# Kernel optimization log

Measured on AMD Instinct MI355X. Metric: run time of the kernel, lower is better.

The kernel has to match this reference:

```python
import jax, jax.numpy as jnp
import numpy as np

B, S, D = 4096, 10, 1024

def setup_inputs() -> dict:
    key = jax.random.key(0)
    ks = jax.random.split(key, 8)
    sD = 1.0 / np.sqrt(D)
    s2D = 1.0 / np.sqrt(2 * D)
    sH = 1.0 / np.sqrt(D // 2)
    return {
        "input_1": jax.random.normal(ks[0], (B, S, D), jnp.float32),
        "input_2": jax.random.normal(ks[1], (B, S, D), jnp.float32),
        # mlp_graph: Linear(2D -> D), stored (in, out)
        "Wg": jax.random.uniform(ks[2], (2 * D, D), jnp.float32, -s2D, s2D),
        "bg": jax.random.uniform(ks[3], (D,), jnp.float32, -s2D, s2D),
        # fd: Linear(2D -> D//2)
        "Wfd": jax.random.uniform(ks[4], (2 * D, D // 2), jnp.float32, -s2D, s2D),
        "bfd": jax.random.uniform(ks[5], (D // 2,), jnp.float32, -s2D, s2D),
        # ff: Linear(D//2 -> 1)
        "Wff": jax.random.uniform(ks[6], (D // 2, 1), jnp.float32, -sH, sH),
        "bff": jax.random.uniform(ks[7], (1,), jnp.float32, -sH, sH),
    }

def reference(input_1, input_2, Wg, bg, Wfd, bfd, Wff, bff):
    # graph_match: cross-graph affinity [B, S, T]
    a = jnp.einsum('bsd,btd->bst', input_1, input_2)
    a_x = jax.nn.softmax(a, axis=1)   # softmax over rows (dim=1)
    a_y = jax.nn.softmax(a, axis=0)   # unusual cross-batch softmax (dim=0)
    # attention_x = a_x^T @ input_1 ; attention_y = a_y @ input_2
    attention_x = jnp.einsum('bst,bsd->btd', a_x, input_1)
    attention_y = jnp.einsum('bst,btd->bsd', a_y, input_2)
    output_x = jnp.concatenate([input_1, attention_y], axis=2) @ Wg + bg
    output_y = jnp.concatenate([input_2, attention_x], axis=2) @ Wg + bg
    # training head: last token of each, concat, fd-ReLU-ff-Sigmoid
    o1 = output_x[:, -1, :]
    o2 = output_y[:, -1, :]
    h = jax.nn.relu(jnp.concatenate([o1, o2], axis=1) @ Wfd + bfd)
    logits = jnp.squeeze(h @ Wff + bff, axis=-1)
    return jax.nn.sigmoid(logits)
```

## Files before the change

kernel.cpp:

```cpp
#include <hip/hip_runtime.h>
#include <hip/hip_bf16.h>

#define BATCH 4096
#define SEQ 10
#define DIM 1024
#define TWOD 2048
#define HID 512

typedef __attribute__((ext_vector_type(8))) short bf16x8;
typedef __attribute__((ext_vector_type(4))) float f32x4;

#define OFF_ABF   0ull
#define OFF_OCB   (32ull << 20)
#define OFF_WGT   (48ull << 20)
#define OFF_WFDT  (52ull << 20)
#define OFF_LOG   (54ull << 20)
#define OFF_AROW  (62ull << 20)
#define OFF_STATS (OFF_AROW + 4096ull * 16 * 4)

#define GLOAD_LDS16(g, l)                                                     \
  __builtin_amdgcn_global_load_lds(                                           \
      (const __attribute__((address_space(1))) unsigned int*)(g),             \
      (__attribute__((address_space(3))) unsigned int*)(l), 16, 0, 0)

#define SW(r) (((r) + ((r) >> 2)) & 3)

static __device__ inline void store_bf4(__hip_bfloat16* p, float4 v) {
  ushort4 u;
  __hip_bfloat16 a = __float2bfloat16(v.x), b = __float2bfloat16(v.y),
                 c = __float2bfloat16(v.z), d = __float2bfloat16(v.w);
  u.x = *(unsigned short*)&a; u.y = *(unsigned short*)&b;
  u.z = *(unsigned short*)&c; u.w = *(unsigned short*)&d;
  *(ushort4*)p = u;
}

__global__ __launch_bounds__(256) void k_scores(
    const float* __restrict__ X1, const float* __restrict__ X2,
    __hip_bfloat16* __restrict__ abf, float* __restrict__ arow,
    float* __restrict__ logits) {
  int b = blockIdx.x;
  int tid = threadIdx.x;
  int wave = tid >> 6, lane = tid & 63;
  const float* x1b = X1 + (size_t)b * SEQ * DIM;
  const float* x2b = X2 + (size_t)b * SEQ * DIM;
  __shared__ float sc[20];
  __shared__ float4 xch[4 * 64];
  if (tid == 0) logits[b] = 0.f;

  const float* Abase;
  const float* Brow;
  if (wave == 0)      { Abase = x1b;           Brow = x2b + 9 * DIM; }
  else if (wave == 1) { Abase = x1b + 5 * DIM; Brow = x2b + 9 * DIM; }
  else if (wave == 2) { Abase = x2b;           Brow = x1b + 9 * DIM; }
  else                { Abase = x2b + 5 * DIM; Brow = x1b + 9 * DIM; }

  float4 ra[5][4], rb[4];
#pragma unroll
  for (int i = 0; i < 4; i++)
    rb[i] = *(const float4*)(Brow + i * 256 + lane * 4);
#pragma unroll
  for (int s = 0; s < 5; s++)
#pragma unroll
    for (int i = 0; i < 4; i++)
      ra[s][i] = *(const float4*)(Abase + s * DIM + i * 256 + lane * 4);

  float v[5];
#pragma unroll
  for (int s = 0; s < 5; s++) {
    float4 a4 = ra[s][0] * rb[0] + ra[s][1] * rb[1] + ra[s][2] * rb[2] +
                ra[s][3] * rb[3];
    v[s] = a4.x + a4.y + a4.z + a4.w;
  }
#pragma unroll
  for (int off = 1; off < 64; off <<= 1)
#pragma unroll
    for (int s = 0; s < 5; s++) v[s] += __shfl_xor(v[s], off, 64);

  if (lane == 0) {
    int base = wave * 5;
    sc[base + 0] = v[0]; sc[base + 1] = v[1]; sc[base + 2] = v[2];
    sc[base + 3] = v[3]; sc[base + 4] = v[4];
  }
  __syncthreads();

  if (tid < SEQ) arow[(size_t)b * 16 + tid] = sc[10 + tid];

  float px[SEQ];
#pragma unroll
  for (int s = 0; s < SEQ; s++) px[s] = sc[s];
  float m = -1e30f;
#pragma unroll
  for (int s = 0; s < SEQ; s++) m = fmaxf(m, px[s]);
  float w[SEQ], Z = 0.f;
#pragma unroll
  for (int s = 0; s < SEQ; s++) { w[s] = __expf(px[s] - m); Z += w[s]; }
  float inv = 1.f / Z;

  __hip_bfloat16* rowx1 = abf + (size_t)b * TWOD;
  __hip_bfloat16* rowx2 = abf + (size_t)(BATCH + b) * TWOD;

  if (wave == 1) {
#pragma unroll
    for (int i = 0; i < 4; i++) {
      float4 pb = ra[0][i] * w[5] + ra[1][i] * w[6] + ra[2][i] * w[7] +
                  ra[3][i] * w[8] + ra[4][i] * w[9];
      xch[i * 64 + lane] = pb;
      store_bf4(rowx2 + i * 256 + lane * 4, rb[i]);
    }
  } else if (wave == 2) {
#pragma unroll
    for (int i = 0; i < 4; i++)
      store_bf4(rowx1 + i * 256 + lane * 4, rb[i]);
  }
  __syncthreads();
  if (wave == 0) {
#pragma unroll
    for (int i = 0; i < 4; i++) {
      float4 ax = ra[0][i] * w[0] + ra[1][i] * w[1] + ra[2][i] * w[2] +
                  ra[3][i] * w[3] + ra[4][i] * w[4];
      ax = (ax + xch[i * 64 + lane]) * inv;
      store_bf4(rowx2 + DIM + i * 256 + lane * 4, ax);
    }
  }
}

__global__ __launch_bounds__(256) void k_stats(const float* __restrict__ arow,
                                               float* __restrict__ stats) {
  int t = blockIdx.x;
  int tid = threadIdx.x, lane = tid & 63, wave = tid >> 6;
  __shared__ float wred[4];
  float m = -1e30f;
  for (int b = tid; b < BATCH; b += 256) m = fmaxf(m, arow[(size_t)b * 16 + t]);
  for (int off = 32; off; off >>= 1) m = fmaxf(m, __shfl_down(m, off, 64));
  if (lane == 0) wred[wave] = m;
  __syncthreads();
  m = fmaxf(fmaxf(wred[0], wred[1]), fmaxf(wred[2], wred[3]));
  __syncthreads();
  float z = 0.f;
  for (int b = tid; b < BATCH; b += 256) z += __expf(arow[(size_t)b * 16 + t] - m);
  for (int off = 32; off; off >>= 1) z += __shfl_down(z, off, 64);
  if (lane == 0) wred[wave] = z;
  __syncthreads();
  if (tid == 0) {
    stats[t] = m;
    stats[16 + t] = wred[0] + wred[1] + wred[2] + wred[3];
  }
}

__global__ __launch_bounds__(256) void k_apply_y(const float* __restrict__ X2,
                                                 const float* __restrict__ arow,
                                                 const float* __restrict__ stats,
                                                 __hip_bfloat16* __restrict__ abf) {
  int b = blockIdx.x;
  int wave = threadIdx.x >> 6, lane = threadIdx.x & 63;
  float wy[SEQ];
#pragma unroll
  for (int t = 0; t < SEQ; t++)
    wy[t] = __expf(arow[(size_t)b * 16 + t] - stats[t]) / stats[16 + t];
  const float* x2b = X2 + (size_t)b * SEQ * DIM;
  int d = wave * 256 + lane * 4;
  float4 acc = {0.f, 0.f, 0.f, 0.f};
#pragma unroll
  for (int t = 0; t < SEQ; t++)
    acc += wy[t] * *(const float4*)(x2b + t * DIM + d);
  store_bf4(abf + (size_t)b * TWOD + DIM + d, acc);
}

__global__ __launch_bounds__(256) void k_transpose_both(
    const float* __restrict__ Wg, const float* __restrict__ Wfd,
    __hip_bfloat16* __restrict__ wgt, __hip_bfloat16* __restrict__ wfdt) {
  __shared__ float t[32][33];
  int by = blockIdx.y;
  const float* in;
  __hip_bfloat16* out;
  int C, c0;
  if (by < 32) { in = Wg; out = wgt; C = DIM; c0 = by * 32; }
  else         { in = Wfd; out = wfdt; C = HID; c0 = (by - 32) * 32; }
  int r0 = blockIdx.x * 32;
  int tx = threadIdx.x & 31, ty = threadIdx.x >> 5;
#pragma unroll
  for (int i = 0; i < 4; i++)
    t[ty + 8 * i][tx] = in[(size_t)(r0 + ty + 8 * i) * C + c0 + tx];
  __syncthreads();
#pragma unroll
  for (int i = 0; i < 4; i++)
    out[(size_t)(c0 + ty + 8 * i) * TWOD + r0 + tx] =
        __float2bfloat16(t[tx][ty + 8 * i]);
}

#define G1_BUF  24576
#define G1_BOFF 16384
#define G1_NT   32

__global__ __launch_bounds__(512, 1) void k_gemm1(
    const __hip_bfloat16* __restrict__ A, const __hip_bfloat16* __restrict__ Bt,
    const float* __restrict__ bias, __hip_bfloat16* __restrict__ outb, int K) {
  __shared__ short lds[3 * G1_BUF];
  int tid = threadIdx.x;
  int lane = tid & 63, wave = tid >> 6;
  int flat = blockIdx.x;
  int swz = (flat & 7) * 32 + (flat >> 3);
  int m0 = (swz >> 3) * 256, n0 = (swz & 7) * 128;
  int wr = wave >> 2, wc = wave & 3;
  int g = lane >> 4, r16 = lane & 15;

  int srow = tid >> 3;
  int ss = (tid & 7) ^ (srow & 7);
  const __hip_bfloat16* sa = A + (size_t)(m0 + srow) * K + ss * 8;
  const __hip_bfloat16* sb = Bt + (size_t)(n0 + srow) * K + ss * 8;
  int dA = wave * 512;
  int dB = G1_BOFF + wave * 512;

#define G1_STAGE(kt, c)                                                       \
  {                                                                           \
    const __hip_bfloat16* sak = sa + (kt)*64;                                 \
    const __hip_bfloat16* sbk = sb + (kt)*64;                                 \
    GLOAD_LDS16(sak + 0 * 64 * K, &lds[(c)*G1_BUF + dA + 0 * 4096]);          \
    GLOAD_LDS16(sak + 1 * 64 * K, &lds[(c)*G1_BUF + dA + 1 * 4096]);          \
    GLOAD_LDS16(sak + 2 * 64 * K, &lds[(c)*G1_BUF + dA + 2 * 4096]);          \
    GLOAD_LDS16(sak + 3 * 64 * K, &lds[(c)*G1_BUF + dA + 3 * 4096]);          \
    GLOAD_LDS16(sbk + 0 * 64 * K, &lds[(c)*G1_BUF + dB + 0 * 4096]);          \
    GLOAD_LDS16(sbk + 1 * 64 * K, &lds[(c)*G1_BUF + dB + 1 * 4096]);          \
  }

  f32x4 acc[8][2] = {};

  G1_STAGE(0, 0);
  G1_STAGE(1, 1);
  asm volatile("s_waitcnt vmcnt(6)" ::: "memory");
  __builtin_amdgcn_sched_barrier(0);
  __builtin_amdgcn_s_barrier();
  __builtin_amdgcn_sched_barrier(0);

#pragma unroll 1
  for (int kt = 0; kt < G1_NT; ++kt) {
    int cur = kt - (kt / 3) * 3;
    if (kt + 2 < G1_NT) {
      int nx = (kt + 2) - ((kt + 2) / 3) * 3;
      G1_STAGE(kt + 2, nx);
    }
    const short* bufA = &lds[cur * G1_BUF];
    const short* bufB = &lds[cur * G1_BUF + G1_BOFF];
#pragma unroll
    for (int kk = 0; kk < 2; ++kk) {
      int sr = ((kk * 4 + g) ^ (r16 & 7)) * 8;
      bf16x8 af[8], bfr[2];
#pragma unroll
      for (int mi = 0; mi < 8; mi++)
        af[mi] = *(const bf16x8*)&bufA[(wr * 128 + mi * 16 + r16) * 64 + sr];
#pragma unroll
      for (int ni = 0; ni < 2; ni++)
        bfr[ni] = *(const bf16x8*)&bufB[(wc * 32 + ni * 16 + r16) * 64 + sr];
      __builtin_amdgcn_s_setprio(1);
#pragma unroll
      for (int mi = 0; mi < 8; mi++)
#pragma unroll
        for (int ni = 0; ni < 2; ni++)
          acc[mi][ni] = __builtin_amdgcn_mfma_f32_16x16x32_bf16(
              af[mi], bfr[ni], acc[mi][ni], 0, 0, 0);
      __builtin_amdgcn_s_setprio(0);
    }
    if (kt < G1_NT - 2)
      asm volatile("s_waitcnt vmcnt(6)" ::: "memory");
    else
      asm volatile("s_waitcnt vmcnt(0)" ::: "memory");
    __builtin_amdgcn_sched_barrier(0);
    __builtin_amdgcn_s_barrier();
    __builtin_amdgcn_sched_barrier(0);
  }

#pragma unroll
  for (int mi = 0; mi < 8; mi++) {
#pragma unroll
    for (int ni = 0; ni < 2; ni++) {
#pragma unroll
      for (int r = 0; r < 4; r++) {
        int m = m0 + wr * 128 + mi * 16 + g * 4 + r;
        int n = n0 + wc * 32 + ni * 16 + r16;
        float v = acc[mi][ni][r] + bias[n];
        int om = m & (BATCH - 1);
        int on = n + ((m >> 12) << 10);
        outb[(size_t)om * TWOD + on] = __float2bfloat16(v);
      }
    }
  }
#undef G1_STAGE
}

#define G2_BUF  12288
#define G2_BOFF 8192
#define G2_NT   32

__global__ __launch_bounds__(256) void k_gemm2_final(
    const __hip_bfloat16* __restrict__ A, const __hip_bfloat16* __restrict__ Bt,
    const float* __restrict__ bfd, const float* __restrict__ Wff,
    float* __restrict__ logits, int K) {
  __shared__ short lds[3 * G2_BUF];
  int tid = threadIdx.x;
  int lane = tid & 63, wave = tid >> 6;
  int flat = blockIdx.x;
  int swz = (flat & 7) * 32 + (flat >> 3);
  int m0 = (swz >> 3) * 128, n0 = (swz & 7) * 64;
  int wr = wave >> 1, wc = wave & 1;
  int g = lane >> 4, r16 = lane & 15;

  int srow = tid >> 3;
  int ss = (tid & 7) ^ (srow & 7);
  const __hip_bfloat16* sa = A + (size_t)(m0 + srow) * K + ss * 8;
  const __hip_bfloat16* sb = Bt + (size_t)(n0 + srow) * K + ss * 8;
  int dA = wave * 512;
  int dB = G2_BOFF + wave * 512;

#define G2_STAGE(kt, c)                                                       \
  {                                                                           \
    const __hip_bfloat16* sak = sa + (kt)*64;                                 \
    const __hip_bfloat16* sbk = sb + (kt)*64;                                 \
    GLOAD_LDS16(sak + 0 * 32 * K, &lds[(c)*G2_BUF + dA + 0 * 2048]);          \
    GLOAD_LDS16(sak + 1 * 32 * K, &lds[(c)*G2_BUF + dA + 1 * 2048]);          \
    GLOAD_LDS16(sak + 2 * 32 * K, &lds[(c)*G2_BUF + dA + 2 * 2048]);          \
    GLOAD_LDS16(sak + 3 * 32 * K, &lds[(c)*G2_BUF + dA + 3 * 2048]);          \
    GLOAD_LDS16(sbk + 0 * 32 * K, &lds[(c)*G2_BUF + dB + 0 * 2048]);          \
    GLOAD_LDS16(sbk + 1 * 32 * K, &lds[(c)*G2_BUF + dB + 1 * 2048]);          \
  }

  f32x4 acc[4][2] = {};

  G2_STAGE(0, 0);
  G2_STAGE(1, 1);
  asm volatile("s_waitcnt vmcnt(6)" ::: "memory");
  __builtin_amdgcn_sched_barrier(0);
  __builtin_amdgcn_s_barrier();
  __builtin_amdgcn_sched_barrier(0);

#pragma unroll 1
  for (int kt = 0; kt < G2_NT; ++kt) {
    int cur = kt - (kt / 3) * 3;
    if (kt + 2 < G2_NT) {
      int nx = (kt + 2) - ((kt + 2) / 3) * 3;
      G2_STAGE(kt + 2, nx);
    }
    const short* bufA = &lds[cur * G2_BUF];
    const short* bufB = &lds[cur * G2_BUF + G2_BOFF];
#pragma unroll
    for (int kk = 0; kk < 2; ++kk) {
      int sr = ((kk * 4 + g) ^ (r16 & 7)) * 8;
      bf16x8 af[4], bfr[2];
#pragma unroll
      for (int mi = 0; mi < 4; mi++)
        af[mi] = *(const bf16x8*)&bufA[(wr * 64 + mi * 16 + r16) * 64 + sr];
#pragma unroll
      for (int ni = 0; ni < 2; ni++)
        bfr[ni] = *(const bf16x8*)&bufB[(wc * 32 + ni * 16 + r16) * 64 + sr];
      __builtin_amdgcn_s_setprio(1);
#pragma unroll
      for (int mi = 0; mi < 4; mi++)
#pragma unroll
        for (int ni = 0; ni < 2; ni++)
          acc[mi][ni] = __builtin_amdgcn_mfma_f32_16x16x32_bf16(
              af[mi], bfr[ni], acc[mi][ni], 0, 0, 0);
      __builtin_amdgcn_s_setprio(0);
    }
    if (kt < G2_NT - 2)
      asm volatile("s_waitcnt vmcnt(6)" ::: "memory");
    else
      asm volatile("s_waitcnt vmcnt(0)" ::: "memory");
    __builtin_amdgcn_sched_barrier(0);
    __builtin_amdgcn_s_barrier();
    __builtin_amdgcn_sched_barrier(0);
  }

  int nA = n0 + wc * 32 + r16, nB = nA + 16;
  float bA = bfd[nA], bB = bfd[nB];
  float wA = Wff[nA], wB = Wff[nB];
#pragma unroll
  for (int mi = 0; mi < 4; mi++) {
#pragma unroll
    for (int r = 0; r < 4; r++) {
      float v0 = acc[mi][0][r] + bA; v0 = v0 > 0.f ? v0 : 0.f;
      float v1 = acc[mi][1][r] + bB; v1 = v1 > 0.f ? v1 : 0.f;
      float pl = v0 * wA + v1 * wB;
#pragma unroll
      for (int off = 1; off < 16; off <<= 1) pl += __shfl_xor(pl, off, 64);
      if (r16 == 0)
        atomicAdd(&logits[m0 + wr * 64 + mi * 16 + g * 4 + r], pl);
    }
  }
#undef G2_STAGE
}

__global__ __launch_bounds__(256) void k_sigmoid(const float* __restrict__ logits,
                                                 const float* __restrict__ bff,
                                                 float* __restrict__ out) {
  int b = blockIdx.x * 256 + threadIdx.x;
  out[b] = 1.f / (1.f + __expf(-(logits[b] + bff[0])));
}

extern "C" void kernel_launch(void* const* d_in, const int* in_sizes, int n_in,
                              void* d_out, int out_size, void* d_ws, size_t ws_size,
                              hipStream_t stream) {
  const float* X1  = (const float*)d_in[0];
  const float* X2  = (const float*)d_in[1];
  const float* Wg  = (const float*)d_in[2];
  const float* bg  = (const float*)d_in[3];
  const float* Wfd = (const float*)d_in[4];
  const float* bfd = (const float*)d_in[5];
  const float* Wff = (const float*)d_in[6];
  const float* bff = (const float*)d_in[7];
  float* out = (float*)d_out;
  char* ws = (char*)d_ws;

  __hip_bfloat16* abf  = (__hip_bfloat16*)(ws + OFF_ABF);
  __hip_bfloat16* ocb  = (__hip_bfloat16*)(ws + OFF_OCB);
  __hip_bfloat16* wgt  = (__hip_bfloat16*)(ws + OFF_WGT);
  __hip_bfloat16* wfdt = (__hip_bfloat16*)(ws + OFF_WFDT);
  float* logits = (float*)(ws + OFF_LOG);
  float* arow   = (float*)(ws + OFF_AROW);
  float* stats  = (float*)(ws + OFF_STATS);

  k_transpose_both<<<dim3(64, 48), 256, 0, stream>>>(Wg, Wfd, wgt, wfdt);
  k_scores<<<BATCH, 256, 0, stream>>>(X1, X2, abf, arow, logits);
  k_stats<<<SEQ, 256, 0, stream>>>(arow, stats);
  k_apply_y<<<BATCH, 256, 0, stream>>>(X2, arow, stats, abf);
  k_gemm1<<<256, 512, 0, stream>>>(abf, wgt, bg, ocb, TWOD);
  k_gemm2_final<<<256, 256, 0, stream>>>(ocb, wfdt, bfd, Wff, logits, TWOD);
  k_sigmoid<<<BATCH / 256, 256, 0, stream>>>(logits, bff, out);
}
```

Measured before the change: 163.2 us.

## Split score kernel into two blocks per batch and stage rows via LDS DMA

The score kernel now launches two blocks per batch element. One block computes the row-wise softmax and attention_x; the other only computes the last-row affinities needed for the cross-batch softmax. Each block stages its 11 input rows into shared memory with direct global-to-LDS loads, instead of keeping them in registers spread across waves. This doubles the number of blocks to raise memory-level parallelism and removes the cross-wave exchange buffer. In exchange it uses about 44KB of LDS per block, which limits how many blocks fit on a CU, and reads the last row of each input twice.

```diff
diff --git a/kernel.cpp b/kernel.cpp
--- a/kernel.cpp
+++ b/kernel.cpp
@@ -38,90 +38,78 @@
     const float* __restrict__ X1, const float* __restrict__ X2,
     __hip_bfloat16* __restrict__ abf, float* __restrict__ arow,
     float* __restrict__ logits) {
-  int b = blockIdx.x;
-  int tid = threadIdx.x;
-  int wave = tid >> 6, lane = tid & 63;
-  const float* x1b = X1 + (size_t)b * SEQ * DIM;
-  const float* x2b = X2 + (size_t)b * SEQ * DIM;
-  __shared__ float sc[20];
-  __shared__ float4 xch[4 * 64];
-  if (tid == 0) logits[b] = 0.f;
-
-  const float* Abase;
-  const float* Brow;
-  if (wave == 0)      { Abase = x1b;           Brow = x2b + 9 * DIM; }
-  else if (wave == 1) { Abase = x1b + 5 * DIM; Brow = x2b + 9 * DIM; }
-  else if (wave == 2) { Abase = x2b;           Brow = x1b + 9 * DIM; }
-  else                { Abase = x2b + 5 * DIM; Brow = x1b + 9 * DIM; }
-
-  float4 ra[5][4], rb[4];
+  __shared__ float X[11 * 1024];
+  __shared__ float sc[12];
+  int role = blockIdx.x & 1;
+  int b = blockIdx.x >> 1;
+  int tid = threadIdx.x, wave = tid >> 6, lane = tid & 63;
+  const float* maj = (role == 0 ? X1 : X2) + (size_t)b * SEQ * DIM;
+  const float* oth = (role == 0 ? X2 : X1) + (size_t)b * SEQ * DIM + 9 * DIM;
+  if (role == 0 && tid == 0) logits[b] = 0.f;
+
+#pragma unroll
+  for (int q = 0; q < 11; q++) {
+    int flat = wave * 11 + q;
+    int r = flat >> 2, c = flat & 3;
+    const float* src = (r < 10) ? (maj + r * DIM) : oth;
+    GLOAD_LDS16(src + c * 256 + lane * 4, &X[r * 1024 + c * 256]);
+  }
+  __syncthreads();
+
+  float4 rb[4];
 #pragma unroll
   for (int i = 0; i < 4; i++)
-    rb[i] = *(const float4*)(Brow + i * 256 + lane * 4);
-#pragma unroll
-  for (int s = 0; s < 5; s++)
-#pragma unroll
-    for (int i = 0; i < 4; i++)
-      ra[s][i] = *(const float4*)(Abase + s * DIM + i * 256 + lane * 4);
-
-  float v[5];
-#pragma unroll
-  for (int s = 0; s < 5; s++) {
-    float4 a4 = ra[s][0] * rb[0] + ra[s][1] * rb[1] + ra[s][2] * rb[2] +
-                ra[s][3] * rb[3];
-    v[s] = a4.x + a4.y + a4.z + a4.w;
+    rb[i] = *(const float4*)&X[10 * 1024 + i * 256 + lane * 4];
+  int scount = (wave < 2) ? 3 : 2;
+  float v[3] = {};
+#pragma unroll
+  for (int j = 0; j < 3; j++) {
+    if (j < scount) {
+      int s = wave + j * 4;
+      float4 a4 = {0.f, 0.f, 0.f, 0.f};
+#pragma unroll
+      for (int i = 0; i < 4; i++) {
+        float4 ra = *(const float4*)&X[s * 1024 + i * 256 + lane * 4];
+        a4 += ra * rb[i];
+      }
+      v[j] = a4.x + a4.y + a4.z + a4.w;
+    }
   }
 #pragma unroll
   for (int off = 1; off < 64; off <<= 1)
 #pragma unroll
-    for (int s = 0; s < 5; s++) v[s] += __shfl_xor(v[s], off, 64);
-
+    for (int j = 0; j < 3; j++) v[j] += __shfl_xor(v[j], off, 64);
   if (lane == 0) {
-    int base = wave * 5;
-    sc[base + 0] = v[0]; sc[base + 1] = v[1]; sc[base + 2] = v[2];
-    sc[base + 3] = v[3]; sc[base + 4] = v[4];
-  }
-  __syncthreads();
-
-  if (tid < SEQ) arow[(size_t)b * 16 + tid] = sc[10 + tid];
-
-  float px[SEQ];
-#pragma unroll
-  for (int s = 0; s < SEQ; s++) px[s] = sc[s];
+#pragma unroll
+    for (int j = 0; j < 3; j++)
+      if (j < scount) sc[wave + j * 4] = v[j];
+  }
+  __syncthreads();
+
+  if (role == 1) {
+    if (tid < SEQ) arow[(size_t)b * 16 + tid] = sc[tid];
+    return;
+  }
+
   float m = -1e30f;
 #pragma unroll
-  for (int s = 0; s < SEQ; s++) m = fmaxf(m, px[s]);
+  for (int s = 0; s < SEQ; s++) m = fmaxf(m, sc[s]);
   float w[SEQ], Z = 0.f;
 #pragma unroll
-  for (int s = 0; s < SEQ; s++) { w[s] = __expf(px[s] - m); Z += w[s]; }
+  for (int s = 0; s < SEQ; s++) { w[s] = __expf(sc[s] - m); Z += w[s]; }
   float inv = 1.f / Z;
 
   __hip_bfloat16* rowx1 = abf + (size_t)b * TWOD;
   __hip_bfloat16* rowx2 = abf + (size_t)(BATCH + b) * TWOD;
-
-  if (wave == 1) {
-#pragma unroll
-    for (int i = 0; i < 4; i++) {
-      float4 pb = ra[0][i] * w[5] + ra[1][i] * w[6] + ra[2][i] * w[7] +
-                  ra[3][i] * w[8] + ra[4][i] * w[9];
-      xch[i * 64 + lane] = pb;
-      store_bf4(rowx2 + i * 256 + lane * 4, rb[i]);
-    }
-  } else if (wave == 2) {
-#pragma unroll
-    for (int i = 0; i < 4; i++)
-      store_bf4(rowx1 + i * 256 + lane * 4, rb[i]);
-  }
-  __syncthreads();
-  if (wave == 0) {
-#pragma unroll
-    for (int i = 0; i < 4; i++) {
-      float4 ax = ra[0][i] * w[0] + ra[1][i] * w[1] + ra[2][i] * w[2] +
-                  ra[3][i] * w[3] + ra[4][i] * w[4];
-      ax = (ax + xch[i * 64 + lane]) * inv;
-      store_bf4(rowx2 + DIM + i * 256 + lane * 4, ax);
-    }
-  }
+  int d = wave * 256 + lane * 4;
+  float4 ax = {0.f, 0.f, 0.f, 0.f};
+#pragma unroll
+  for (int s = 0; s < SEQ; s++)
+    ax += w[s] * *(const float4*)&X[s * 1024 + d];
+  ax *= inv;
+  store_bf4(rowx2 + DIM + d, ax);
+  store_bf4(rowx1 + d, *(const float4*)&X[9 * 1024 + d]);
+  store_bf4(rowx2 + d, *(const float4*)&X[10 * 1024 + d]);
 }
 
 __global__ __launch_bounds__(256) void k_stats(const float* __restrict__ arow,
@@ -418,7 +406,7 @@
   float* stats  = (float*)(ws + OFF_STATS);
 
   k_transpose_both<<<dim3(64, 48), 256, 0, stream>>>(Wg, Wfd, wgt, wfdt);
-  k_scores<<<BATCH, 256, 0, stream>>>(X1, X2, abf, arow, logits);
+  k_scores<<<2 * BATCH, 256, 0, stream>>>(X1, X2, abf, arow, logits);
   k_stats<<<SEQ, 256, 0, stream>>>(arow, stats);
   k_apply_y<<<BATCH, 256, 0, stream>>>(X2, arow, stats, abf);
   k_gemm1<<<256, 512, 0, stream>>>(abf, wgt, bg, ocb, TWOD);
```

Result: no change. 164.8 us (+1.0%).
